# Kernel tuning notes

Measured on AMD Instinct MI355X. Metric: run time of the kernel, lower is better.

The kernel has to match this reference:

```python
import jax, jax.numpy as jnp
import numpy as np

B, N, G, K, V = 4, 512, 8, 64, 32000


def setup_inputs() -> dict:
    key = jax.random.key(0)
    k1, k2, k3 = jax.random.split(key, 3)
    phi = jax.random.normal(k1, (B, N, G, K), dtype=jnp.float32)
    # psi initialized uniform(-0.5, 0.5) as in torch.nn.init.uniform_
    psi = jax.random.uniform(k2, (V, K), dtype=jnp.float32, minval=-0.5, maxval=0.5)
    # perm[h, v] = index of h^{-1} acting on vocab word v (data-dependent permutation)
    perm = jax.random.randint(k3, (G, V), 0, V, dtype=jnp.int64)
    return {"phi": phi, "psi": psi, "perm": perm}


def reference(phi, psi, perm):
    # For each group element h: logits[b,n,v] += dot(phi[b,n,h,:], psi[perm[h,v],:])
    # Gather psi rows per group element: [G, V, K]
    psi_g = psi[perm]
    logits = jnp.einsum("bnhk,hvk->bnv", phi, psi_g)  # [B, N, V]
    return jax.nn.softmax(logits, axis=-1)
```

## Files before the change

### kernel.cpp

```cpp
#include <hip/hip_runtime.h>
#include <math.h>


#define M_ROWS 2048
#define V_DIM  32000
#define C_DIM  512
#define G_DIM  8
#define K_DIM  64
#define BM     128
#define BV     128
#define BK     32
#define NVBLK  (V_DIM / BV)
#define NMT    (M_ROWS / BM)
#define NKT    (C_DIM / BK)
#define NSEG   25
#define SEGV   (NVBLK / NSEG)
#define LDSBUF 12288
#define LDS_ROW 40

typedef _Float16 f16x8 __attribute__((ext_vector_type(8)));
typedef _Float16 f16x4 __attribute__((ext_vector_type(4)));
typedef float    f32x4 __attribute__((ext_vector_type(4)));


__device__ __forceinline__ void gl_lds16(const void* g, void* l) {
  __builtin_amdgcn_global_load_lds(
      (const __attribute__((address_space(1))) unsigned int*)g,
      (__attribute__((address_space(3))) unsigned int*)l, 16, 0, 0);
}

__global__ __launch_bounds__(256) void gdecode_prep_phi(
    const float* __restrict__ phi, _Float16* __restrict__ aws)
{
  const int ga   = blockIdx.x * 256 + threadIdx.x;
  const int g    = ga & 511;
  const int half = (ga >> 9) & 1;
  const int tile = ga >> 10;
  const int kq = g >> 7, r = g & 127;
  const int m  = (tile >> 4) * BM + r;
  const int k  = (tile & 15) * BK + kq * 8;
  const float4 x0 = *(const float4*)(phi + (size_t)m * C_DIM + k);
  const float4 x1 = *(const float4*)(phi + (size_t)m * C_DIM + k + 4);
  const float xs[8] = {x0.x, x0.y, x0.z, x0.w, x1.x, x1.y, x1.z, x1.w};
  f16x8 o;
  #pragma unroll
  for (int j = 0; j < 8; ++j) {
    _Float16 hi = (_Float16)xs[j];
    o[j] = half ? (_Float16)(xs[j] - (float)hi) : hi;
  }
  *(f16x8*)(aws + (size_t)ga * 8) = o;
}

__global__ __launch_bounds__(256) void gdecode_prep_psi(
    const float* __restrict__ psi, const int* __restrict__ perm, const int pstride,
    _Float16* __restrict__ bws)
{
  const int gb   = blockIdx.x * 256 + threadIdx.x;
  const int g    = gb & 511;
  const int tile = gb >> 9;
  const int it = tile / 250;
  const int vb = tile - it * 250;
  const int kq = g >> 7, r = g & 127;
  const int h   = it >> 1;
  const int kin = (it & 1) * 32 + kq * 8;
  const int v   = vb * BV + r;
  const int pr  = perm[(size_t)(h * V_DIM + v) * pstride];
  const float4 x0 = *(const float4*)(psi + (size_t)pr * K_DIM + kin);
  const float4 x1 = *(const float4*)(psi + (size_t)pr * K_DIM + kin + 4);
  f16x8 o = {(_Float16)x0.x, (_Float16)x0.y, (_Float16)x0.z, (_Float16)x0.w,
             (_Float16)x1.x, (_Float16)x1.y, (_Float16)x1.z, (_Float16)x1.w};
  *(f16x8*)(bws + (size_t)gb * 8) = o;
}

__global__ __launch_bounds__(256, 4) void gdecode_gemm2(
    const _Float16* __restrict__ aws, const _Float16* __restrict__ bws,
    float* __restrict__ out, float* __restrict__ smax, float* __restrict__ ssum)
{
  __shared__ __align__(16) _Float16 lds[2 * LDSBUF];

  const int b   = blockIdx.x;
  const int xcd = b & 7;
  const int i   = b >> 3;
  const int mt  = i >> 5;
  const int vb  = xcd * 32 + (i & 31);
  if (vb >= NVBLK) return;

  const int vbase = vb * BV;
  const int mbase = mt * BM;

  const int t    = threadIdx.x;
  const int wid  = t >> 6;
  const int lane = t & 63;
  const int wm   = wid & 1;
  const int wv   = wid >> 1;
  const int lrow = lane & 15;
  const int quad = lane >> 4;

  const _Float16* gA = aws + (size_t)mt * NKT * 2 * 4096;
  const _Float16* gB = bws + (size_t)vb * 4096;

  auto STAGE = [&](int it, _Float16* dst) {
    const _Float16* ga = gA + (size_t)it * 2 * 4096;
    const _Float16* gb = gB + (size_t)it * NVBLK * 4096;
    gl_lds16(ga + (size_t)t * 8,          dst + t * 8);
    gl_lds16(ga + 2048 + (size_t)t * 8,   dst + 2048 + t * 8);
    gl_lds16(ga + 4096 + (size_t)t * 8,   dst + 4096 + t * 8);
    gl_lds16(ga + 6144 + (size_t)t * 8,   dst + 6144 + t * 8);
    gl_lds16(gb + (size_t)t * 8,          dst + 8192 + t * 8);
    gl_lds16(gb + 2048 + (size_t)t * 8,   dst + 8192 + 2048 + t * 8);
  };

  f32x4 acc[4][4] = {};

  STAGE(0, lds);
  __syncthreads();

  for (int it = 0; it < 16; ++it) {
    _Float16* cur = lds + (it & 1) * LDSBUF;
    if (it < 15) STAGE(it + 1, lds + ((it & 1) ^ 1) * LDSBUF);

    const _Float16* sAh = cur;
    const _Float16* sAl = cur + 4096;
    const _Float16* sB  = cur + 8192;

    f16x8 ah[4], al[4], bf[4];
    #pragma unroll
    for (int k = 0; k < 4; ++k) {
      const int ra = quad * 1024 + (wm * 64 + k * 16 + lrow) * 8;
      const int rb = quad * 1024 + (wv * 64 + k * 16 + lrow) * 8;
      ah[k] = *(const f16x8*)(sAh + ra);
      al[k] = *(const f16x8*)(sAl + ra);
      bf[k] = *(const f16x8*)(sB + rb);
    }
    #pragma unroll
    for (int k = 0; k < 4; ++k) {
      #pragma unroll
      for (int j = 0; j < 4; ++j) {
        acc[k][j] = __builtin_amdgcn_mfma_f32_16x16x32_f16(ah[k], bf[j], acc[k][j], 0, 0, 0);
        acc[k][j] = __builtin_amdgcn_mfma_f32_16x16x32_f16(al[k], bf[j], acc[k][j], 0, 0, 0);
      }
    }
    __syncthreads();
  }

  float* redmax = (float*)lds;
  float* redsum = redmax + 2 * BM;
  const int rowb = wm * 64;

  #pragma unroll
  for (int k = 0; k < 4; ++k) {
    #pragma unroll
    for (int r = 0; r < 4; ++r) {
      float v = fmaxf(fmaxf(acc[k][0][r], acc[k][1][r]),
                      fmaxf(acc[k][2][r], acc[k][3][r]));
      v = fmaxf(v, __shfl_xor(v, 1));
      v = fmaxf(v, __shfl_xor(v, 2));
      v = fmaxf(v, __shfl_xor(v, 4));
      v = fmaxf(v, __shfl_xor(v, 8));
      if (lrow == 0) redmax[(rowb + k * 16 + quad * 4 + r) * 2 + wv] = v;
    }
  }
  __syncthreads();
  float gmx[4][4];
  #pragma unroll
  for (int k = 0; k < 4; ++k) {
    #pragma unroll
    for (int r = 0; r < 4; ++r) {
      int row = rowb + k * 16 + quad * 4 + r;
      gmx[k][r] = fmaxf(redmax[row * 2], redmax[row * 2 + 1]);
    }
  }
  #pragma unroll
  for (int k = 0; k < 4; ++k) {
    #pragma unroll
    for (int r = 0; r < 4; ++r) {
      float s = __expf(acc[k][0][r] - gmx[k][r]) + __expf(acc[k][1][r] - gmx[k][r])
              + __expf(acc[k][2][r] - gmx[k][r]) + __expf(acc[k][3][r] - gmx[k][r]);
      s += __shfl_xor(s, 1);
      s += __shfl_xor(s, 2);
      s += __shfl_xor(s, 4);
      s += __shfl_xor(s, 8);
      if (lrow == 0) redsum[(rowb + k * 16 + quad * 4 + r) * 2 + wv] = s;
    }
  }
  __syncthreads();
  if (t < BM) {
    size_t o = (size_t)vb * M_ROWS + mbase + t;
    smax[o] = fmaxf(redmax[t * 2], redmax[t * 2 + 1]);
    ssum[o] = redsum[t * 2] + redsum[t * 2 + 1];
  }
  #pragma unroll
  for (int k = 0; k < 4; ++k) {
    #pragma unroll
    for (int j = 0; j < 4; ++j) {
      #pragma unroll
      for (int r = 0; r < 4; ++r) {
        int grow = mbase + rowb + k * 16 + quad * 4 + r;
        int gcol = vbase + wv * 64 + j * 16 + lrow;
        __builtin_nontemporal_store(acc[k][j][r], out + (size_t)grow * V_DIM + gcol);
      }
    }
  }
}

__global__ __launch_bounds__(256) void gdecode_combine1(
    const float* __restrict__ smax, const float* __restrict__ ssum,
    float* __restrict__ pmax, float* __restrict__ psum)
{
  const int seg = blockIdx.x % NSEG;
  const int m   = (blockIdx.x / NSEG) * 256 + threadIdx.x;
  float Mv = -3.4e38f;
  #pragma unroll
  for (int j = 0; j < SEGV; ++j)
    Mv = fmaxf(Mv, smax[(size_t)(seg * SEGV + j) * M_ROWS + m]);
  float S = 0.f;
  #pragma unroll
  for (int j = 0; j < SEGV; ++j) {
    const size_t o = (size_t)(seg * SEGV + j) * M_ROWS + m;
    S += ssum[o] * __expf(smax[o] - Mv);
  }
  pmax[(size_t)seg * M_ROWS + m] = Mv;
  psum[(size_t)seg * M_ROWS + m] = S;
}

__global__ __launch_bounds__(256) void gdecode_combine2(
    const float* __restrict__ pmax, const float* __restrict__ psum,
    float* __restrict__ rowM, float* __restrict__ rowI)
{
  const int m = blockIdx.x * 256 + threadIdx.x;
  float Mv = -3.4e38f;
  #pragma unroll
  for (int s = 0; s < NSEG; ++s) Mv = fmaxf(Mv, pmax[(size_t)s * M_ROWS + m]);
  float S = 0.f;
  #pragma unroll
  for (int s = 0; s < NSEG; ++s)
    S += psum[(size_t)s * M_ROWS + m] * __expf(pmax[(size_t)s * M_ROWS + m] - Mv);
  rowM[m] = Mv;
  rowI[m] = 1.f / S;
}

__global__ __launch_bounds__(256) void gdecode_norm(
    float* __restrict__ out, const float* __restrict__ rowM, const float* __restrict__ rowI)
{
  const int m = blockIdx.x >> 2;
  const int c = blockIdx.x & 3;
  const float Mv = rowM[m];
  const float Iv = rowI[m];
  f32x4* row = (f32x4*)(out + (size_t)m * V_DIM + c * 8000);
  for (int i = threadIdx.x; i < 2000; i += 256) {
    f32x4 x = row[i];
    f32x4 y;
    y[0] = __expf(x[0] - Mv) * Iv;
    y[1] = __expf(x[1] - Mv) * Iv;
    y[2] = __expf(x[2] - Mv) * Iv;
    y[3] = __expf(x[3] - Mv) * Iv;
    __builtin_nontemporal_store(y, row + i);
  }
}


__global__ __launch_bounds__(256, 2) void gdecode_gemm_fb(
    const float* __restrict__ phi, const float* __restrict__ psi,
    const int* __restrict__ perm, const int pstride,
    float* __restrict__ out, float* __restrict__ smax, float* __restrict__ ssum)
{
  __shared__ __align__(16) _Float16 lds[3 * BM * LDS_ROW];
  _Float16* sAhi = lds;
  _Float16* sAlo = lds + BM * LDS_ROW;
  _Float16* sB   = lds + 2 * BM * LDS_ROW;

  const int t     = threadIdx.x;
  const int vbase = blockIdx.x * BV;
  const int mbase = blockIdx.y * BM;

  const int kg = t & 7;
  const int r0 = t >> 3;

  const int wid  = t >> 6;
  const int lane = t & 63;
  const int wm   = wid & 1;
  const int wv   = wid >> 1;
  const int lrow = lane & 15;
  const int quad = lane >> 4;

  f32x4 acc[4][4] = {};

  for (int it = 0; it < 16; ++it) {
    const int cb  = it * BK;
    const int h   = cb >> 6;
    const int kin = cb & 63;

    float4 av[4], bv[4];
    #pragma unroll
    for (int i = 0; i < 4; ++i) {
      int m = r0 + i * 32;
      av[i] = *(const float4*)(phi + (size_t)(mbase + m) * C_DIM + cb + kg * 4);
    }
    #pragma unroll
    for (int i = 0; i < 4; ++i) {
      int v  = r0 + i * 32;
      int pr = perm[(size_t)(h * V_DIM + vbase + v) * pstride];
      bv[i]  = *(const float4*)(psi + (size_t)pr * K_DIM + kin + kg * 4);
    }

    __syncthreads();

    #pragma unroll
    for (int i = 0; i < 4; ++i) {
      int m = r0 + i * 32;
      float4 x = av[i];
      _Float16 h0 = (_Float16)x.x, h1 = (_Float16)x.y,
               h2 = (_Float16)x.z, h3 = (_Float16)x.w;
      f16x4 hi = {h0, h1, h2, h3};
      f16x4 lo = {(_Float16)(x.x - (float)h0), (_Float16)(x.y - (float)h1),
                  (_Float16)(x.z - (float)h2), (_Float16)(x.w - (float)h3)};
      *(f16x4*)(sAhi + m * LDS_ROW + kg * 4) = hi;
      *(f16x4*)(sAlo + m * LDS_ROW + kg * 4) = lo;
    }
    #pragma unroll
    for (int i = 0; i < 4; ++i) {
      int v = r0 + i * 32;
      float4 x = bv[i];
      f16x4 w = {(_Float16)x.x, (_Float16)x.y, (_Float16)x.z, (_Float16)x.w};
      *(f16x4*)(sB + v * LDS_ROW + kg * 4) = w;
    }

    __syncthreads();

    f16x8 ah[4], al[4], bf[4];
    #pragma unroll
    for (int i = 0; i < 4; ++i) {
      ah[i] = *(const f16x8*)(sAhi + (wm * 64 + i * 16 + lrow) * LDS_ROW + quad * 8);
      al[i] = *(const f16x8*)(sAlo + (wm * 64 + i * 16 + lrow) * LDS_ROW + quad * 8);
      bf[i] = *(const f16x8*)(sB   + (wv * 64 + i * 16 + lrow) * LDS_ROW + quad * 8);
    }
    #pragma unroll
    for (int i = 0; i < 4; ++i) {
      #pragma unroll
      for (int j = 0; j < 4; ++j) {
        acc[i][j] = __builtin_amdgcn_mfma_f32_16x16x32_f16(ah[i], bf[j], acc[i][j], 0, 0, 0);
        acc[i][j] = __builtin_amdgcn_mfma_f32_16x16x32_f16(al[i], bf[j], acc[i][j], 0, 0, 0);
      }
    }
  }

  __syncthreads();
  float* redmax = (float*)lds;
  float* redsum = redmax + 2 * BM;
  const int rowb = wm * 64;

  #pragma unroll
  for (int i = 0; i < 4; ++i) {
    #pragma unroll
    for (int r = 0; r < 4; ++r) {
      float v = fmaxf(fmaxf(acc[i][0][r], acc[i][1][r]),
                      fmaxf(acc[i][2][r], acc[i][3][r]));
      v = fmaxf(v, __shfl_xor(v, 1));
      v = fmaxf(v, __shfl_xor(v, 2));
      v = fmaxf(v, __shfl_xor(v, 4));
      v = fmaxf(v, __shfl_xor(v, 8));
      if (lrow == 0) redmax[(rowb + i * 16 + quad * 4 + r) * 2 + wv] = v;
    }
  }
  __syncthreads();
  float gmx[4][4];
  #pragma unroll
  for (int i = 0; i < 4; ++i) {
    #pragma unroll
    for (int r = 0; r < 4; ++r) {
      int row = rowb + i * 16 + quad * 4 + r;
      gmx[i][r] = fmaxf(redmax[row * 2], redmax[row * 2 + 1]);
    }
  }
  #pragma unroll
  for (int i = 0; i < 4; ++i) {
    #pragma unroll
    for (int r = 0; r < 4; ++r) {
      float s = __expf(acc[i][0][r] - gmx[i][r]) + __expf(acc[i][1][r] - gmx[i][r])
              + __expf(acc[i][2][r] - gmx[i][r]) + __expf(acc[i][3][r] - gmx[i][r]);
      s += __shfl_xor(s, 1);
      s += __shfl_xor(s, 2);
      s += __shfl_xor(s, 4);
      s += __shfl_xor(s, 8);
      if (lrow == 0) redsum[(rowb + i * 16 + quad * 4 + r) * 2 + wv] = s;
    }
  }
  __syncthreads();
  if (smax != nullptr && t < BM) {
    int row = t;
    size_t o = (size_t)(mbase + row) * NVBLK + blockIdx.x;
    smax[o] = fmaxf(redmax[row * 2], redmax[row * 2 + 1]);
    ssum[o] = redsum[row * 2] + redsum[row * 2 + 1];
  }
  #pragma unroll
  for (int i = 0; i < 4; ++i) {
    #pragma unroll
    for (int j = 0; j < 4; ++j) {
      #pragma unroll
      for (int r = 0; r < 4; ++r) {
        int grow = mbase + rowb + i * 16 + quad * 4 + r;
        int gcol = vbase + wv * 64 + j * 16 + lrow;
        out[(size_t)grow * V_DIM + gcol] = acc[i][j][r];
      }
    }
  }
}

__global__ __launch_bounds__(256) void gdecode_softmax_ws(
    float* __restrict__ out, const float* __restrict__ smax, const float* __restrict__ ssum)
{
  __shared__ float sbuf[4];
  const int m = blockIdx.x;
  const int t = threadIdx.x;
  const float* rm = smax + (size_t)m * NVBLK;
  const float* rs = ssum + (size_t)m * NVBLK;

  float lm = -3.4e38f;
  for (int i = t; i < NVBLK; i += 256) lm = fmaxf(lm, rm[i]);
  for (int d = 1; d < 64; d <<= 1) lm = fmaxf(lm, __shfl_xor(lm, d));
  if ((t & 63) == 0) sbuf[t >> 6] = lm;
  __syncthreads();
  const float M = fmaxf(fmaxf(sbuf[0], sbuf[1]), fmaxf(sbuf[2], sbuf[3]));
  __syncthreads();

  float ls = 0.f;
  for (int i = t; i < NVBLK; i += 256) ls += rs[i] * __expf(rm[i] - M);
  for (int d = 1; d < 64; d <<= 1) ls += __shfl_xor(ls, d);
  if ((t & 63) == 0) sbuf[t >> 6] = ls;
  __syncthreads();
  const float inv = 1.f / (sbuf[0] + sbuf[1] + sbuf[2] + sbuf[3]);

  float4* row = (float4*)(out + (size_t)m * V_DIM);
  for (int i = t; i < V_DIM / 4; i += 256) {
    float4 x = row[i];
    x.x = __expf(x.x - M) * inv;
    x.y = __expf(x.y - M) * inv;
    x.z = __expf(x.z - M) * inv;
    x.w = __expf(x.w - M) * inv;
    row[i] = x;
  }
}

__global__ __launch_bounds__(256) void gdecode_softmax_nows(float* __restrict__ out)
{
  __shared__ float sbuf[4];
  const int m = blockIdx.x;
  const int t = threadIdx.x;
  float4* row = (float4*)(out + (size_t)m * V_DIM);

  float lm = -3.4e38f;
  for (int i = t; i < V_DIM / 4; i += 256) {
    float4 x = row[i];
    lm = fmaxf(lm, fmaxf(fmaxf(x.x, x.y), fmaxf(x.z, x.w)));
  }
  for (int d = 1; d < 64; d <<= 1) lm = fmaxf(lm, __shfl_xor(lm, d));
  if ((t & 63) == 0) sbuf[t >> 6] = lm;
  __syncthreads();
  const float M = fmaxf(fmaxf(sbuf[0], sbuf[1]), fmaxf(sbuf[2], sbuf[3]));
  __syncthreads();

  float ls = 0.f;
  for (int i = t; i < V_DIM / 4; i += 256) {
    float4 x = row[i];
    ls += __expf(x.x - M) + __expf(x.y - M) + __expf(x.z - M) + __expf(x.w - M);
  }
  for (int d = 1; d < 64; d <<= 1) ls += __shfl_xor(ls, d);
  if ((t & 63) == 0) sbuf[t >> 6] = ls;
  __syncthreads();
  const float inv = 1.f / (sbuf[0] + sbuf[1] + sbuf[2] + sbuf[3]);

  for (int i = t; i < V_DIM / 4; i += 256) {
    float4 x = row[i];
    x.x = __expf(x.x - M) * inv;
    x.y = __expf(x.y - M) * inv;
    x.z = __expf(x.z - M) * inv;
    x.w = __expf(x.w - M) * inv;
    row[i] = x;
  }
}


extern "C" void kernel_launch(void* const* d_in, const int* in_sizes, int n_in,
                              void* d_out, int out_size, void* d_ws, size_t ws_size,
                              hipStream_t stream)
{
  const float* phi  = (const float*)d_in[0];
  const float* psi  = (const float*)d_in[1];
  const int*   perm = (const int*)d_in[2];
  const int pstride = (in_sizes[2] == 2 * G_DIM * V_DIM) ? 2 : 1;

  float* out = (float*)d_out;

  const size_t AWS_B  = (size_t)NMT * NKT * 2 * 4096 * 2;
  const size_t BWS_B  = (size_t)NKT * NVBLK * 4096 * 2;
  const size_t STAT_B = (size_t)NVBLK * M_ROWS * 4;
  const size_t PART_B = (size_t)NSEG * M_ROWS * 4;
  const size_t ROW_B  = (size_t)M_ROWS * 4;
  const size_t need_fast = AWS_B + BWS_B + 2 * STAT_B + 2 * PART_B + 2 * ROW_B;

  if (d_ws != nullptr && ws_size >= need_fast) {
    char* wp = (char*)d_ws;
    _Float16* aws = (_Float16*)wp;                 wp += AWS_B;
    _Float16* bws = (_Float16*)wp;                 wp += BWS_B;
    float* smax   = (float*)wp;                    wp += STAT_B;
    float* ssum   = (float*)wp;                    wp += STAT_B;
    float* pmax   = (float*)wp;                    wp += PART_B;
    float* psum   = (float*)wp;                    wp += PART_B;
    float* rowM   = (float*)wp;                    wp += ROW_B;
    float* rowI   = (float*)wp;

    gdecode_prep_phi<<<(NMT * NKT * 2 * 512) / 256, 256, 0, stream>>>(phi, aws);
    gdecode_prep_psi<<<(NKT * NVBLK * 512) / 256, 256, 0, stream>>>(psi, perm, pstride, bws);

    gdecode_gemm2<<<4096, 256, 0, stream>>>(aws, bws, out, smax, ssum);

    gdecode_combine1<<<NSEG * (M_ROWS / 256), 256, 0, stream>>>(smax, ssum, pmax, psum);
    gdecode_combine2<<<M_ROWS / 256, 256, 0, stream>>>(pmax, psum, rowM, rowI);
    gdecode_norm<<<M_ROWS * 4, 256, 0, stream>>>(out, rowM, rowI);
    return;
  }

  const size_t need_old = (size_t)M_ROWS * NVBLK * 2 * sizeof(float);
  const bool hasws = (d_ws != nullptr) && (ws_size >= need_old);
  float* smax = hasws ? (float*)d_ws : nullptr;
  float* ssum = hasws ? smax + (size_t)M_ROWS * NVBLK : nullptr;

  dim3 grid(NVBLK, M_ROWS / BM);
  gdecode_gemm_fb<<<grid, 256, 0, stream>>>(phi, psi, perm, pstride, out, smax, ssum);

  if (hasws)
    gdecode_softmax_ws<<<M_ROWS, 256, 0, stream>>>(out, smax, ssum);
  else
    gdecode_softmax_nows<<<M_ROWS, 256, 0, stream>>>(out);
}
```

Measured before the change: 542.8 us.

## Deepen GEMM LDS prefetch to two stages and fold combine2 into norm kernel

The GEMM main loop now issues loads two iterations ahead and waits with explicit vmcnt and lgkmcnt counters plus raw barriers, instead of staging one tile ahead under full __syncthreads. This lets global-to-LDS loads overlap more compute. Separately, the second combine kernel is folded into the normalization kernel: each block recomputes its row max and sum from the 25 partials. That removes one launch and the rowM/rowI round trip at the cost of redundant small reductions per block. The hand-written waitcnt values depend on exactly six outstanding loads per stage and are fragile if the compiler reorders them.

After: 543.8 us. Within noise of the previous version (+0.2%).

```diff
diff --git a/kernel.cpp b/kernel.cpp
--- a/kernel.cpp
+++ b/kernel.cpp
@@ -113,11 +113,15 @@
   f32x4 acc[4][4] = {};
 
   STAGE(0, lds);
-  __syncthreads();
-
+  STAGE(1, lds + LDSBUF);
+
+  #pragma unroll 2
   for (int it = 0; it < 16; ++it) {
     _Float16* cur = lds + (it & 1) * LDSBUF;
-    if (it < 15) STAGE(it + 1, lds + ((it & 1) ^ 1) * LDSBUF);
+
+    if (it < 15) asm volatile("s_waitcnt vmcnt(6)" ::: "memory");
+    else         asm volatile("s_waitcnt vmcnt(0)" ::: "memory");
+    __builtin_amdgcn_s_barrier();
 
     const _Float16* sAh = cur;
     const _Float16* sAl = cur + 4096;
@@ -140,7 +144,9 @@
         acc[k][j] = __builtin_amdgcn_mfma_f32_16x16x32_f16(al[k], bf[j], acc[k][j], 0, 0, 0);
       }
     }
-    __syncthreads();
+    asm volatile("s_waitcnt lgkmcnt(0)" ::: "memory");
+    __builtin_amdgcn_s_barrier();
+    if (it < 14) STAGE(it + 2, cur);
   }
 
   float* redmax = (float*)lds;
@@ -223,11 +229,11 @@
   psum[(size_t)seg * M_ROWS + m] = S;
 }
 
-__global__ __launch_bounds__(256) void gdecode_combine2(
-    const float* __restrict__ pmax, const float* __restrict__ psum,
-    float* __restrict__ rowM, float* __restrict__ rowI)
-{
-  const int m = blockIdx.x * 256 + threadIdx.x;
+__global__ __launch_bounds__(256) void gdecode_norm(
+    float* __restrict__ out, const float* __restrict__ pmax, const float* __restrict__ psum)
+{
+  const int m = blockIdx.x >> 2;
+  const int c = blockIdx.x & 3;
   float Mv = -3.4e38f;
   #pragma unroll
   for (int s = 0; s < NSEG; ++s) Mv = fmaxf(Mv, pmax[(size_t)s * M_ROWS + m]);
@@ -235,20 +241,11 @@
   #pragma unroll
   for (int s = 0; s < NSEG; ++s)
     S += psum[(size_t)s * M_ROWS + m] * __expf(pmax[(size_t)s * M_ROWS + m] - Mv);
-  rowM[m] = Mv;
-  rowI[m] = 1.f / S;
-}
-
-__global__ __launch_bounds__(256) void gdecode_norm(
-    float* __restrict__ out, const float* __restrict__ rowM, const float* __restrict__ rowI)
-{
-  const int m = blockIdx.x >> 2;
-  const int c = blockIdx.x & 3;
-  const float Mv = rowM[m];
-  const float Iv = rowI[m];
+  const float Iv = 1.f / S;
+
   f32x4* row = (f32x4*)(out + (size_t)m * V_DIM + c * 8000);
   for (int i = threadIdx.x; i < 2000; i += 256) {
-    f32x4 x = row[i];
+    f32x4 x = __builtin_nontemporal_load(row + i);
     f32x4 y;
     y[0] = __expf(x[0] - Mv) * Iv;
     y[1] = __expf(x[1] - Mv) * Iv;
@@ -495,8 +492,7 @@
   const size_t BWS_B  = (size_t)NKT * NVBLK * 4096 * 2;
   const size_t STAT_B = (size_t)NVBLK * M_ROWS * 4;
   const size_t PART_B = (size_t)NSEG * M_ROWS * 4;
-  const size_t ROW_B  = (size_t)M_ROWS * 4;
-  const size_t need_fast = AWS_B + BWS_B + 2 * STAT_B + 2 * PART_B + 2 * ROW_B;
+  const size_t need_fast = AWS_B + BWS_B + 2 * STAT_B + 2 * PART_B;
 
   if (d_ws != nullptr && ws_size >= need_fast) {
     char* wp = (char*)d_ws;
@@ -505,9 +501,7 @@
     float* smax   = (float*)wp;                    wp += STAT_B;
     float* ssum   = (float*)wp;                    wp += STAT_B;
     float* pmax   = (float*)wp;                    wp += PART_B;
-    float* psum   = (float*)wp;                    wp += PART_B;
-    float* rowM   = (float*)wp;                    wp += ROW_B;
-    float* rowI   = (float*)wp;
+    float* psum   = (float*)wp;
 
     gdecode_prep_phi<<<(NMT * NKT * 2 * 512) / 256, 256, 0, stream>>>(phi, aws);
     gdecode_prep_psi<<<(NKT * NVBLK * 512) / 256, 256, 0, stream>>>(psi, perm, pstride, bws);
@@ -515,8 +509,7 @@
     gdecode_gemm2<<<4096, 256, 0, stream>>>(aws, bws, out, smax, ssum);
 
     gdecode_combine1<<<NSEG * (M_ROWS / 256), 256, 0, stream>>>(smax, ssum, pmax, psum);
-    gdecode_combine2<<<M_ROWS / 256, 256, 0, stream>>>(pmax, psum, rowM, rowI);
-    gdecode_norm<<<M_ROWS * 4, 256, 0, stream>>>(out, rowM, rowI);
+    gdecode_norm<<<M_ROWS * 4, 256, 0, stream>>>(out, pmax, psum);
     return;
   }
 
```
